# Kernel tuning notes

Hardware: AMD Instinct MI355X
Metric: run time of the kernel (lower is better)

Reference implementation:

```python
import jax, jax.numpy as jnp
import numpy as np

B, T, I, H, L = 256, 512, 64, 256, 2


def _lstm_layer(x, Wih, Whh, bih, bhh):
    # x: [B, T, Din]; Wih: [4H, Din]; Whh: [4H, H]; gate order i,f,g,o (PyTorch)
    Hdim = Whh.shape[1]
    # Precompute input projections for all timesteps (one big GEMM)
    x_proj = jnp.einsum('btd,gd->btg', x, Wih) + bih + bhh  # [B, T, 4H]
    x_proj = jnp.transpose(x_proj, (1, 0, 2))  # [T, B, 4H]

    def step(carry, xt):
        h, c = carry
        gates = xt + h @ Whh.T  # [B, 4H]
        i, f, g, o = jnp.split(gates, 4, axis=-1)
        i = jax.nn.sigmoid(i)
        f = jax.nn.sigmoid(f)
        g = jnp.tanh(g)
        o = jax.nn.sigmoid(o)
        c = f * c + i * g
        h = o * jnp.tanh(c)
        return (h, c), h

    b = x.shape[0]
    h0 = jnp.zeros((b, Hdim), dtype=x.dtype)
    c0 = jnp.zeros((b, Hdim), dtype=x.dtype)
    _, hs = jax.lax.scan(step, (h0, c0), x_proj)  # hs: [T, B, H]
    return jnp.transpose(hs, (1, 0, 2))  # [B, T, H]


def setup_inputs() -> dict:
    key = jax.random.key(0)
    ks = jax.random.split(key, 12)
    s_in = 1.0 / np.sqrt(H)
    inp = {
        'x': jax.random.normal(ks[0], (B, T, I), dtype=jnp.float32),
        'Wih0': jax.random.uniform(ks[1], (4 * H, I), minval=-s_in, maxval=s_in),
        'Whh0': jax.random.uniform(ks[2], (4 * H, H), minval=-s_in, maxval=s_in),
        'bih0': jax.random.uniform(ks[3], (4 * H,), minval=-s_in, maxval=s_in),
        'bhh0': jax.random.uniform(ks[4], (4 * H,), minval=-s_in, maxval=s_in),
        'Wih1': jax.random.uniform(ks[5], (4 * H, H), minval=-s_in, maxval=s_in),
        'Whh1': jax.random.uniform(ks[6], (4 * H, H), minval=-s_in, maxval=s_in),
        'bih1': jax.random.uniform(ks[7], (4 * H,), minval=-s_in, maxval=s_in),
        'bhh1': jax.random.uniform(ks[8], (4 * H,), minval=-s_in, maxval=s_in),
        'Wfc': jax.random.uniform(ks[9], (1, H), minval=-s_in, maxval=s_in),
        'bfc': jax.random.uniform(ks[10], (1,), minval=-s_in, maxval=s_in),
    }
    return inp


def reference(x, Wih0, Whh0, bih0, bhh0, Wih1, Whh1, bih1, bhh1, Wfc, bfc):
    h1 = _lstm_layer(x, Wih0, Whh0, bih0, bhh0)   # [B, T, H]
    h2 = _lstm_layer(h1, Wih1, Whh1, bih1, bhh1)  # [B, T, H]
    last = h2[:, -1, :]                           # [B, H]
    return last @ Wfc.T + bfc                     # [B, 1]
```

## Files before the change

### kernel.cpp

```cpp
#include <hip/hip_runtime.h>

#define TT   512
#define IDIM 64
#define HDIM 256

typedef short  short8  __attribute__((ext_vector_type(8)));
typedef short  short4v __attribute__((ext_vector_type(4)));
typedef float  f32x4   __attribute__((ext_vector_type(4)));
typedef unsigned long long u64;

__device__ __forceinline__ short f2bf(float f) {
    unsigned u = __float_as_uint(f);
    u = u + 0x7FFFu + ((u >> 16) & 1u);
    return (short)(u >> 16);
}
__device__ __forceinline__ float bf2f(short h) {
    return __uint_as_float(((unsigned)(unsigned short)h) << 16);
}
__device__ __forceinline__ float sigm(float x)  { return 1.0f / (1.0f + __expf(-x)); }
__device__ __forceinline__ float tanh_(float x) { return 2.0f / (1.0f + __expf(-2.0f * x)) - 1.0f; }

__device__ __forceinline__ void unpack16(const u64 W[6], u64 q[4]) {
    unsigned short u[16];
#pragma unroll
    for (int w = 0; w < 6; ++w)
#pragma unroll
        for (int k = 0; k < 3; ++k) {
            int j = 3 * w + k;
            if (j < 16) u[j] = (unsigned short)(W[w] >> (16 * k));
        }
#pragma unroll
    for (int t = 0; t < 4; ++t)
        q[t] = (u64)u[4*t] | ((u64)u[4*t+1] << 16) | ((u64)u[4*t+2] << 32) | ((u64)u[4*t+3] << 48);
}

__global__ __launch_bounds__(256, 1) void lstm_fused(
    const float* __restrict__ x,
    const float* __restrict__ Wih0, const float* __restrict__ Whh0,
    const float* __restrict__ bih0, const float* __restrict__ bhh0,
    const float* __restrict__ Wih1, const float* __restrict__ Whh1,
    const float* __restrict__ bih1, const float* __restrict__ bhh1,
    const float* __restrict__ Wfc,  const float* __restrict__ bfc,
    float* __restrict__ out, char* __restrict__ ws)
{
    u64* h0buf = (u64*)ws;
    u64* h1buf = h0buf + 2 * 16 * 16 * 96;

    const int blk   = blockIdx.x;
    const int grp   = ((blk & 7) << 1) | ((blk >> 3) & 1);
    const int chunk = blk >> 4;
    const int tid   = threadIdx.x;
    const int lane  = tid & 63;
    const int wave  = tid >> 6;
    const int quad  = lane >> 4;
    const int nn    = lane & 15;

    __shared__ short A0[16][328];
    __shared__ short A1[16][520];
    __shared__ float gbuf[2][4][16][17];
    __shared__ float red[16][16];
    __shared__ float ldspad[5120];

    for (int i = tid; i < 16 * 328; i += 256) (&A0[0][0])[i] = 0;
    for (int i = tid; i < 16 * 520; i += 256) (&A1[0][0])[i] = 0;

    const int wrow = wave * HDIM + chunk * 16 + nn;
    short8 w0f[10];
    short8 w1f[16];
#pragma unroll
    for (int kb = 0; kb < 10; ++kb)
#pragma unroll
        for (int j = 0; j < 8; ++j) {
            int k = kb * 32 + quad * 8 + j;
            float v = (k < 64) ? Wih0[wrow * IDIM + k] : Whh0[wrow * HDIM + (k - 64)];
            w0f[kb][j] = f2bf(v);
        }
#pragma unroll
    for (int kb = 0; kb < 16; ++kb)
#pragma unroll
        for (int j = 0; j < 8; ++j) {
            int k = kb * 32 + quad * 8 + j;
            float v = (k < 256) ? Wih1[wrow * HDIM + k] : Whh1[wrow * HDIM + (k - 256)];
            w1f[kb][j] = f2bf(v);
        }
    const float bias0 = bih0[wrow] + bhh0[wrow];
    const float bias1 = bih1[wrow] + bhh1[wrow];

    const int em = tid >> 4;
    const int ej = tid & 15;
    float c0 = 0.0f, c1 = 0.0f;

    auto load_x = [&](int t) {
        const float4 v = *(const float4*)&x[((size_t)(grp * 16 + em) * TT + t) * IDIM + ej * 4];
        short4v sv;
        sv[0] = f2bf(v.x); sv[1] = f2bf(v.y); sv[2] = f2bf(v.z); sv[3] = f2bf(v.w);
        *(short4v*)&A0[em][ej * 4] = sv;
    };

    __syncthreads();
    load_x(0);
    __syncthreads();

    for (int s = 0; s <= TT; ++s) {
        if (s < TT) {
            f32x4 accA = {0.f, 0.f, 0.f, 0.f}, accB = {0.f, 0.f, 0.f, 0.f};
#pragma unroll
            for (int kb = 0; kb < 10; kb += 2) {
                short8 a0v = *(const short8*)&A0[nn][kb * 32 + quad * 8];
                short8 a1v = *(const short8*)&A0[nn][(kb + 1) * 32 + quad * 8];
                accA = __builtin_amdgcn_mfma_f32_16x16x32_bf16(a0v, w0f[kb],     accA, 0, 0, 0);
                accB = __builtin_amdgcn_mfma_f32_16x16x32_bf16(a1v, w0f[kb + 1], accB, 0, 0, 0);
            }
            const f32x4 acc = accA + accB;
#pragma unroll
            for (int r = 0; r < 4; ++r)
                gbuf[0][wave][quad * 4 + r][nn] = acc[r] + bias0;
        }
        __syncthreads();

        if (s < TT) {
            float gi = sigm (gbuf[0][0][em][ej]);
            float gf = sigm (gbuf[0][1][em][ej]);
            float gg = tanh_(gbuf[0][2][em][ej]);
            float go = sigm (gbuf[0][3][em][ej]);
            c0 = gf * c0 + gi * gg;
            const short h0v = f2bf(go * tanh_(c0));
            const int hv = (int)(unsigned short)h0v;
            const int n1 = __shfl_down(hv, 1);
            const int n2 = __shfl_down(hv, 2);
            if ((ej % 3) == 0) {
                const int w = ej / 3;
                u64 v0 = (u64)(unsigned)(s + 1) << 48;
                v0 |= (u64)(unsigned)hv;
                if (w < 5) {
                    v0 |= (u64)(unsigned)n1 << 16;
                    v0 |= (u64)(unsigned)n2 << 32;
                }
                const size_t base = (((size_t)(s & 1) * 16 + grp) * 16 + em) * 96
                                    + chunk * 6 + w;
                (void)__hip_atomic_exchange(&h0buf[base], v0,
                                            __ATOMIC_RELAXED, __HIP_MEMORY_SCOPE_AGENT);
            }
        }

        if (s >= 1) {
            f32x4 accA = {0.f, 0.f, 0.f, 0.f}, accB = {0.f, 0.f, 0.f, 0.f};
#pragma unroll
            for (int kb = 0; kb < 16; kb += 2) {
                short8 a0v = *(const short8*)&A1[nn][kb * 32 + quad * 8];
                short8 a1v = *(const short8*)&A1[nn][(kb + 1) * 32 + quad * 8];
                accA = __builtin_amdgcn_mfma_f32_16x16x32_bf16(a0v, w1f[kb],     accA, 0, 0, 0);
                accB = __builtin_amdgcn_mfma_f32_16x16x32_bf16(a1v, w1f[kb + 1], accB, 0, 0, 0);
            }
            const f32x4 acc = accA + accB;
#pragma unroll
            for (int r = 0; r < 4; ++r)
                gbuf[1][wave][quad * 4 + r][nn] = acc[r] + bias1;
        }
        __syncthreads();

        {
            short h1v = 0;
            if (s >= 1) {
                float gi = sigm (gbuf[1][0][em][ej]);
                float gf = sigm (gbuf[1][1][em][ej]);
                float gg = tanh_(gbuf[1][2][em][ej]);
                float go = sigm (gbuf[1][3][em][ej]);
                c1 = gf * c1 + gi * gg;
                h1v = f2bf(go * tanh_(c1));
            }
            const int hv = (int)(unsigned short)h1v;
            const int n1 = __shfl_down(hv, 1);
            const int n2 = __shfl_down(hv, 2);
            if ((ej % 3) == 0) {
                const int w = ej / 3;
                u64 v1 = (u64)(unsigned)(s + 1) << 48;
                v1 |= (u64)(unsigned)hv;
                if (w < 5) {
                    v1 |= (u64)(unsigned)n1 << 16;
                    v1 |= (u64)(unsigned)n2 << 32;
                }
                const size_t base = (((size_t)(s & 1) * 16 + grp) * 16 + em) * 96
                                    + chunk * 6 + w;
                (void)__hip_atomic_exchange(&h1buf[base], v1,
                                            __ATOMIC_RELAXED, __HIP_MEMORY_SCOPE_AGENT);
            }
        }

        if (s + 1 < TT) load_x(s + 1);

        {
            const bool g0 = (s < TT), g1 = (s >= 1);
            const unsigned sq = (unsigned)(s + 1);
            const size_t rb = (((size_t)(s & 1) * 16 + grp) * 16 + em) * 96 + ej * 6;
            u64 W0[6], W1[6];
            bool ok0 = !g0, ok1 = !g1;
            int budget = 1 << 17;
            while ((!ok0 || !ok1) && budget-- > 0) {
                if (!ok0) {
#pragma unroll
                    for (int i = 0; i < 6; ++i)
                        W0[i] = __hip_atomic_load(&h0buf[rb + i],
                                                  __ATOMIC_RELAXED, __HIP_MEMORY_SCOPE_AGENT);
                    bool t = true;
#pragma unroll
                    for (int i = 0; i < 6; ++i) t &= ((unsigned)(W0[i] >> 48) == sq);
                    ok0 = t;
                }
                if (!ok1) {
#pragma unroll
                    for (int i = 0; i < 6; ++i)
                        W1[i] = __hip_atomic_load(&h1buf[rb + i],
                                                  __ATOMIC_RELAXED, __HIP_MEMORY_SCOPE_AGENT);
                    bool t = true;
#pragma unroll
                    for (int i = 0; i < 6; ++i) t &= ((unsigned)(W1[i] >> 48) == sq);
                    ok1 = t;
                }
            }
            asm volatile("s_waitcnt vmcnt(0)" ::: "memory");

            if (g0) {
                u64 q[4]; unpack16(W0, q);
                u64* d0 = (u64*)&A0[em][64 + ej * 16];
                u64* d1 = (u64*)&A1[em][ej * 16];
#pragma unroll
                for (int t = 0; t < 4; ++t) { d0[t] = q[t]; d1[t] = q[t]; }
            }
            if (g1) {
                u64 q[4]; unpack16(W1, q);
                u64* d2 = (u64*)&A1[em][256 + ej * 16];
#pragma unroll
                for (int t = 0; t < 4; ++t) d2[t] = q[t];
            }
        }
        __syncthreads();
    }

    {
        float part = 0.f;
#pragma unroll
        for (int kk = 0; kk < 16; ++kk) {
            int k = ej * 16 + kk;
            part += bf2f(A1[em][256 + k]) * Wfc[k];
        }
        red[em][ej] = part;
    }
    __syncthreads();
    if (chunk == 0 && tid < 16) {
        float sum = bfc[0];
#pragma unroll
        for (int c = 0; c < 16; ++c) sum += red[tid][c];
        out[grp * 16 + tid] = sum;
    }

    if (gridDim.x > 100000) { ldspad[tid] = bias0; out[0] = ldspad[255 - tid]; }
}

extern "C" void kernel_launch(void* const* d_in, const int* in_sizes, int n_in,
                              void* d_out, int out_size, void* d_ws, size_t ws_size,
                              hipStream_t stream) {
    (void)in_sizes; (void)n_in; (void)out_size; (void)ws_size;
    const float* x    = (const float*)d_in[0];
    const float* Wih0 = (const float*)d_in[1];
    const float* Whh0 = (const float*)d_in[2];
    const float* bih0 = (const float*)d_in[3];
    const float* bhh0 = (const float*)d_in[4];
    const float* Wih1 = (const float*)d_in[5];
    const float* Whh1 = (const float*)d_in[6];
    const float* bih1 = (const float*)d_in[7];
    const float* bhh1 = (const float*)d_in[8];
    const float* Wfc  = (const float*)d_in[9];
    const float* bfc  = (const float*)d_in[10];

    lstm_fused<<<256, 256, 0, stream>>>(x, Wih0, Whh0, bih0, bhh0,
                                        Wih1, Whh1, bih1, bhh1, Wfc, bfc,
                                        (float*)d_out, (char*)d_ws);
}
```

Baseline: 1.659 ms.

## Defer layer-1 hidden-state exchange wait to overlap with layer-0 gate math

The cross-block wait for the layer-1 hidden state is moved from the end of each step to just before the layer-1 matmul of the next step. Its loads are issued before the layer-0 activations, so the exchange latency can hide behind that work, and the end-of-step spin now waits only on layer-0 data. A final wait after the loop collects the last layer-1 state. This adds one extra __syncthreads per step and more complex sequence-number bookkeeping.

```diff
diff --git a/kernel.cpp b/kernel.cpp
--- a/kernel.cpp
+++ b/kernel.cpp
@@ -118,30 +118,64 @@
         }
         __syncthreads();
 
-        if (s < TT) {
-            float gi = sigm (gbuf[0][0][em][ej]);
-            float gf = sigm (gbuf[0][1][em][ej]);
-            float gg = tanh_(gbuf[0][2][em][ej]);
-            float go = sigm (gbuf[0][3][em][ej]);
-            c0 = gf * c0 + gi * gg;
-            const short h0v = f2bf(go * tanh_(c0));
-            const int hv = (int)(unsigned short)h0v;
-            const int n1 = __shfl_down(hv, 1);
-            const int n2 = __shfl_down(hv, 2);
-            if ((ej % 3) == 0) {
-                const int w = ej / 3;
-                u64 v0 = (u64)(unsigned)(s + 1) << 48;
-                v0 |= (u64)(unsigned)hv;
-                if (w < 5) {
-                    v0 |= (u64)(unsigned)n1 << 16;
-                    v0 |= (u64)(unsigned)n2 << 32;
+        {
+            const bool gh1 = (s >= 2);
+            const unsigned sq1 = (unsigned)s;
+            const size_t rb1 = (((size_t)((s - 1) & 1) * 16 + grp) * 16 + em) * 96 + ej * 6;
+            u64 W1[6];
+            if (gh1) {
+#pragma unroll
+                for (int i = 0; i < 6; ++i)
+                    W1[i] = __hip_atomic_load(&h1buf[rb1 + i],
+                                              __ATOMIC_RELAXED, __HIP_MEMORY_SCOPE_AGENT);
+            }
+
+            if (s < TT) {
+                float gi = sigm (gbuf[0][0][em][ej]);
+                float gf = sigm (gbuf[0][1][em][ej]);
+                float gg = tanh_(gbuf[0][2][em][ej]);
+                float go = sigm (gbuf[0][3][em][ej]);
+                c0 = gf * c0 + gi * gg;
+                const short h0v = f2bf(go * tanh_(c0));
+                const int hv = (int)(unsigned short)h0v;
+                const int n1 = __shfl_down(hv, 1);
+                const int n2 = __shfl_down(hv, 2);
+                if ((ej % 3) == 0) {
+                    const int w = ej / 3;
+                    u64 v0 = (u64)(unsigned)(s + 1) << 48;
+                    v0 |= (u64)(unsigned)hv;
+                    if (w < 5) {
+                        v0 |= (u64)(unsigned)n1 << 16;
+                        v0 |= (u64)(unsigned)n2 << 32;
+                    }
+                    const size_t base = (((size_t)(s & 1) * 16 + grp) * 16 + em) * 96
+                                        + chunk * 6 + w;
+                    (void)__hip_atomic_exchange(&h0buf[base], v0,
+                                                __ATOMIC_RELAXED, __HIP_MEMORY_SCOPE_AGENT);
                 }
-                const size_t base = (((size_t)(s & 1) * 16 + grp) * 16 + em) * 96
-                                    + chunk * 6 + w;
-                (void)__hip_atomic_exchange(&h0buf[base], v0,
-                                            __ATOMIC_RELAXED, __HIP_MEMORY_SCOPE_AGENT);
-            }
-        }
+            }
+
+            if (gh1) {
+                bool ok = true;
+#pragma unroll
+                for (int i = 0; i < 6; ++i) ok &= ((unsigned)(W1[i] >> 48) == sq1);
+                int budget = 1 << 17;
+                while (!ok && budget-- > 0) {
+#pragma unroll
+                    for (int i = 0; i < 6; ++i)
+                        W1[i] = __hip_atomic_load(&h1buf[rb1 + i],
+                                                  __ATOMIC_RELAXED, __HIP_MEMORY_SCOPE_AGENT);
+                    ok = true;
+#pragma unroll
+                    for (int i = 0; i < 6; ++i) ok &= ((unsigned)(W1[i] >> 48) == sq1);
+                }
+                u64 q[4]; unpack16(W1, q);
+                u64* d2 = (u64*)&A1[em][256 + ej * 16];
+#pragma unroll
+                for (int t = 0; t < 4; ++t) d2[t] = q[t];
+            }
+        }
+        __syncthreads();
 
         if (s >= 1) {
             f32x4 accA = {0.f, 0.f, 0.f, 0.f}, accB = {0.f, 0.f, 0.f, 0.f};
@@ -190,52 +224,55 @@
         if (s + 1 < TT) load_x(s + 1);
 
         {
-            const bool g0 = (s < TT), g1 = (s >= 1);
+            const bool g0 = (s < TT);
             const unsigned sq = (unsigned)(s + 1);
             const size_t rb = (((size_t)(s & 1) * 16 + grp) * 16 + em) * 96 + ej * 6;
-            u64 W0[6], W1[6];
-            bool ok0 = !g0, ok1 = !g1;
-            int budget = 1 << 17;
-            while ((!ok0 || !ok1) && budget-- > 0) {
-                if (!ok0) {
+            if (g0) {
+                u64 W0[6];
+                bool ok0 = false;
+                int budget = 1 << 17;
+                do {
 #pragma unroll
                     for (int i = 0; i < 6; ++i)
                         W0[i] = __hip_atomic_load(&h0buf[rb + i],
                                                   __ATOMIC_RELAXED, __HIP_MEMORY_SCOPE_AGENT);
-                    bool t = true;
-#pragma unroll
-                    for (int i = 0; i < 6; ++i) t &= ((unsigned)(W0[i] >> 48) == sq);
-                    ok0 = t;
-                }
-                if (!ok1) {
-#pragma unroll
-                    for (int i = 0; i < 6; ++i)
-                        W1[i] = __hip_atomic_load(&h1buf[rb + i],
-                                                  __ATOMIC_RELAXED, __HIP_MEMORY_SCOPE_AGENT);
-                    bool t = true;
-#pragma unroll
-                    for (int i = 0; i < 6; ++i) t &= ((unsigned)(W1[i] >> 48) == sq);
-                    ok1 = t;
-                }
-            }
-            asm volatile("s_waitcnt vmcnt(0)" ::: "memory");
-
-            if (g0) {
+                    ok0 = true;
+#pragma unroll
+                    for (int i = 0; i < 6; ++i) ok0 &= ((unsigned)(W0[i] >> 48) == sq);
+                } while (!ok0 && budget-- > 0);
+
                 u64 q[4]; unpack16(W0, q);
                 u64* d0 = (u64*)&A0[em][64 + ej * 16];
                 u64* d1 = (u64*)&A1[em][ej * 16];
 #pragma unroll
                 for (int t = 0; t < 4; ++t) { d0[t] = q[t]; d1[t] = q[t]; }
             }
-            if (g1) {
-                u64 q[4]; unpack16(W1, q);
-                u64* d2 = (u64*)&A1[em][256 + ej * 16];
-#pragma unroll
-                for (int t = 0; t < 4; ++t) d2[t] = q[t];
-            }
+            asm volatile("s_waitcnt vmcnt(0)" ::: "memory");
         }
         __syncthreads();
     }
+
+    {
+        const unsigned sq = (unsigned)(TT + 1);
+        const size_t rb = (((size_t)(TT & 1) * 16 + grp) * 16 + em) * 96 + ej * 6;
+        u64 W1[6];
+        bool ok = false;
+        int budget = 1 << 17;
+        do {
+#pragma unroll
+            for (int i = 0; i < 6; ++i)
+                W1[i] = __hip_atomic_load(&h1buf[rb + i],
+                                          __ATOMIC_RELAXED, __HIP_MEMORY_SCOPE_AGENT);
+            ok = true;
+#pragma unroll
+            for (int i = 0; i < 6; ++i) ok &= ((unsigned)(W1[i] >> 48) == sq);
+        } while (!ok && budget-- > 0);
+        u64 q[4]; unpack16(W1, q);
+        u64* d2 = (u64*)&A1[em][256 + ej * 16];
+#pragma unroll
+        for (int t = 0; t < 4; ++t) d2[t] = q[t];
+    }
+    __syncthreads();
 
     {
         float part = 0.f;
```

Measured after the change: 1.622 ms. 2.2% less time.
